# Performance work log

Hardware: AMD Instinct MI355X
Metric: run time of the kernel (lower is better)

## Reference

```python
import jax, jax.numpy as jnp
import numpy as np

NUM_BLOCKS = 2
RES_LAYERS = 10
RC, DC, SC, EC, OC, GC = 32, 32, 1024, 512, 256, 5
RF = NUM_BLOCKS * (2 ** RES_LAYERS - 1)  # receptive/residual field = 2046


def _conv(x, w, dil, pad_left):
    # x: (N, C, L), w: (O, I, K). Causal: left pad only (equivalent to
    # torch padding=d followed by slicing off the last d samples).
    return jax.lax.conv_general_dilated(
        x, w, window_strides=(1,), padding=[(pad_left, 0)],
        rhs_dilation=(dil,), dimension_numbers=('NCH', 'OIH', 'NCH'))


def setup_inputs() -> dict:
    key = jax.random.key(0)
    ks = jax.random.split(key, 13)
    B, L = 2, 8192
    nl = NUM_BLOCKS * RES_LAYERS
    s = lambda k, shape, sc: (jax.random.normal(k, shape, jnp.float32) * sc)
    return {
        'inputs': s(ks[0], (B, 256, L), 1.0),
        'conditioning': s(ks[1], (B, GC), 1.0),
        'input_w': s(ks[2], (RC, 256, 1), 0.06),
        'filter_w': s(ks[3], (nl, DC, RC, 2), 0.12),
        'gate_w': s(ks[4], (nl, DC, RC, 2), 0.12),
        'res_w': s(ks[5], (nl, RC, DC, 1), 0.17),
        'split_w': s(ks[6], (nl, SC, DC, 1), 0.17),
        'gcf_w': s(ks[7], (nl, 1, GC), 0.3),
        'gcs_w': s(ks[8], (nl, 1, GC), 0.3),
        'f1_w': s(ks[9], (EC, SC, 1), 0.03),
        'f1_b': jnp.zeros((EC,), jnp.float32),
        'f2_w': s(ks[10], (OC, EC, 1), 0.04),
        'f2_b': jnp.zeros((OC,), jnp.float32),
    }


def reference(inputs, conditioning, input_w, filter_w, gate_w, res_w,
              split_w, gcf_w, gcs_w, f1_w, f1_b, f2_w, f2_b):
    L = inputs.shape[2]
    tgt = L - RF  # target_length
    res = _conv(inputs, input_w, 1, 0)  # (B, RC, L)
    final = jnp.zeros((inputs.shape[0], SC, tgt), inputs.dtype)
    for b in range(NUM_BLOCKS):
        for l in range(RES_LAYERS):
            i = b * RES_LAYERS + l
            d = 2 ** l
            f = _conv(res, filter_w[i], d, d)  # causal dilated, length L
            g = _conv(res, gate_w[i], d, d)
            # global conditioning: Linear(GC,1) -> per-batch scalar, broadcast
            gc_f = (conditioning @ gcf_w[i].T)[:, None, :]  # (B,1,1)
            gc_g = (conditioning @ gcs_w[i].T)[:, None, :]
            out = jnp.tanh(f + gc_f) * jax.nn.sigmoid(g + gc_g)
            res = _conv(out, res_w[i], 1, 0) + res
            final = final + _conv(out, split_w[i], 1, 0)[:, :, -tgt:]
    x = jax.nn.relu(final)
    x = _conv(x, f1_w, 1, 0) + f1_b[None, :, None]
    x = jax.nn.relu(x)
    x = _conv(x, f2_w, 1, 0) + f2_b[None, :, None]
    n, c, ln = x.shape
    return jnp.transpose(x, (0, 2, 1)).reshape(n * ln, c)
```

## Files before the change

kernel.cpp:

```cpp
#include <hip/hip_runtime.h>
#include <hip/hip_bf16.h>
#include <cstddef>

#define Bc   2
#define Lc   8192
#define TGT  6146
#define NL   20
#define RCc  32
#define DCc  32
#define SCc  1024
#define ECc  512
#define OCc  256
#define KTOT (NL * DCc)
#define TTILES 49

typedef __attribute__((ext_vector_type(4))) float f32x4;
typedef __attribute__((ext_vector_type(8))) short bf16x8;
typedef __attribute__((ext_vector_type(4))) int i32x4;
typedef __attribute__((ext_vector_type(2))) int i32x2;

typedef __attribute__((address_space(1))) void* as1v;
typedef __attribute__((address_space(3))) void* as3v;

__device__ inline bf16x8 cvt8(const float4* p) {
    float4 a = p[0], b = p[1];
    union { bf16x8 v; __hip_bfloat16 h[8]; } u;
    u.h[0] = __float2bfloat16(a.x); u.h[1] = __float2bfloat16(a.y);
    u.h[2] = __float2bfloat16(a.z); u.h[3] = __float2bfloat16(a.w);
    u.h[4] = __float2bfloat16(b.x); u.h[5] = __float2bfloat16(b.y);
    u.h[6] = __float2bfloat16(b.z); u.h[7] = __float2bfloat16(b.w);
    return u.v;
}

__global__ __launch_bounds__(256) void prep_kernel(
    const float* __restrict__ x,
    const float* __restrict__ iw,
    float* __restrict__ res_out,
    const float* __restrict__ split_w,
    const float* __restrict__ f1_w,
    const float* __restrict__ f2_w,
    const float* __restrict__ filt,
    const float* __restrict__ gate,
    const float* __restrict__ resw,
    __hip_bfloat16* __restrict__ Wp1,
    __hip_bfloat16* __restrict__ Wp2,
    __hip_bfloat16* __restrict__ Wp3,
    __hip_bfloat16* __restrict__ wfgp,
    __hip_bfloat16* __restrict__ wrp,
    int npack)
{
    __shared__ float ws[32][256];
    __shared__ float xs[64][64];
    int tid = threadIdx.x;

    if ((int)blockIdx.x < npack) {
        int idx = blockIdx.x * 256 + tid;
        const int N1 = SCc * KTOT, N2 = ECc * SCc, N3 = OCc * ECc, N4 = NL * 64 * 64;
        if (idx < N1) {
            int m = idx / KTOT, k = idx % KTOT;
            int i = k >> 5, c = k & 31;
            Wp1[idx] = __float2bfloat16(split_w[((size_t)i * SCc + m) * DCc + c]);
            return;
        }
        idx -= N1;
        if (idx < N2) { Wp2[idx] = __float2bfloat16(f1_w[idx]); return; }
        idx -= N2;
        if (idx < N3) { Wp3[idx] = __float2bfloat16(f2_w[idx]); return; }
        idx -= N3;
        if (idx < N4) {
            int li = idx / 4096, r = idx % 4096;
            int m = r >> 6, k = r & 63;
            int tap = k >> 5, ic = k & 31;
            float v = (m < 32) ? filt[(size_t)li * 2048 + (m * 32 + ic) * 2 + tap]
                               : gate[(size_t)li * 2048 + ((m - 32) * 32 + ic) * 2 + tap];
            int slot = (k >> 3) ^ (m & 7);
            wfgp[((size_t)li * 64 + m) * 64 + slot * 8 + (k & 7)] = __float2bfloat16(v);
            if (r < 2048) {
                int m2 = r >> 6;
                float v2 = (k < 32) ? resw[(size_t)li * 1024 + m2 * 32 + k] : 0.f;
                wrp[((size_t)li * 32 + m2) * 64 + slot * 8 + (k & 7)] = __float2bfloat16(v2);
            }
        }
        return;
    }

    int bid = blockIdx.x - npack;
    int b   = bid >> 7;
    int t0  = (bid & 127) * 64;

    for (int idx = tid; idx < 32 * 256; idx += 256)
        ws[idx >> 8][idx & 255] = iw[idx];

    int tl = tid & 63, qq = tid >> 6, oc0 = qq * 8;
    float acc[8] = {};

    for (int icc = 0; icc < 4; ++icc) {
        __syncthreads();
        for (int idx = tid; idx < 64 * 64; idx += 256) {
            int icl = idx >> 6, tll = idx & 63;
            xs[icl][tll] = x[((size_t)b * 256 + icc * 64 + icl) * Lc + t0 + tll];
        }
        __syncthreads();
        for (int icl = 0; icl < 64; icl += 4) {
            float x0 = xs[icl][tl], x1 = xs[icl + 1][tl];
            float x2 = xs[icl + 2][tl], x3 = xs[icl + 3][tl];
#pragma unroll
            for (int j = 0; j < 8; ++j) {
                const float4 w4 = *(const float4*)&ws[oc0 + j][icc * 64 + icl];
                acc[j] += w4.x * x0 + w4.y * x1 + w4.z * x2 + w4.w * x3;
            }
        }
    }
#pragma unroll
    for (int j = 0; j < 8; ++j)
        res_out[((size_t)b * 32 + oc0 + j) * Lc + t0 + tl] = acc[j];
}

__global__ __launch_bounds__(512) void layer_group5(
    const float* __restrict__ res_in,
    float* __restrict__ res_out,
    __hip_bfloat16* __restrict__ outsT,
    const __hip_bfloat16* __restrict__ wfgp,
    const __hip_bfloat16* __restrict__ wrp,
    const float* __restrict__ cond,
    const float* __restrict__ gcf_w,
    const float* __restrict__ gcs_w,
    int l0)
{
    constexpr int W = 96, H = 32, NT = 6;
    __shared__ __align__(16) float resL[W * 36];
    __shared__ __align__(16) unsigned short OsL[W * 40];
    __shared__ __align__(16) i32x4 Wf[2][64 * 8];
    __shared__ __align__(16) i32x4 Wrs[2][32 * 8];

    int tid  = threadIdx.x;
    int b    = blockIdx.y;
    int t0   = blockIdx.x * 64;
    int lane = tid & 63, wid = tid >> 6;
    int r15  = lane & 15, q = lane >> 4;

    const float* rb = res_in + (size_t)b * 32 * Lc;
    for (int idx = tid; idx < W * 32; idx += 512) {
        int ch = idx / W, tl = idx % W;
        int tg = t0 - H + tl;
        resL[tl * 36 + ch] = (tg >= 0) ? rb[(size_t)ch * Lc + tg] : 0.f;
    }

    auto issueW = [&](int bufi, int li2) {
        const __hip_bfloat16* wfg = wfgp + (size_t)li2 * 4096;
        const __hip_bfloat16* wrl = wrp  + (size_t)li2 * 2048;
        __builtin_amdgcn_global_load_lds(
            (as1v)(void*)((const i32x4*)wfg + wid * 64 + lane),
            (as3v)(void*)&Wf[bufi][wid * 64], 16, 0, 0);
        if (wid < 4)
            __builtin_amdgcn_global_load_lds(
                (as1v)(void*)((const i32x4*)wrl + wid * 64 + lane),
                (as3v)(void*)&Wrs[bufi][wid * 64], 16, 0, 0);
    };
    issueW(0, l0);

#pragma unroll
    for (int i = 0; i < 5; ++i) {
        const int cur = i & 1;
        int li = l0 + i;
        int d  = 1 << i;

        float gf = 0.f, gg = 0.f;
#pragma unroll
        for (int c = 0; c < 5; ++c) {
            gf += gcf_w[li * 5 + c] * cond[b * 5 + c];
            gg += gcs_w[li * 5 + c] * cond[b * 5 + c];
        }
        __syncthreads();
        if (i + 1 < 5) issueW(cur ^ 1, li + 1);

        const bf16x8* Wv = (const bf16x8*)Wf[cur];
        for (int tt = wid; tt < NT; tt += 8) {
            int ct0 = tt * 16;
            int srow0 = ct0 + r15 - d; if (srow0 < 0) srow0 = 0;
            int srow1 = ct0 + r15;
            bf16x8 a0 = cvt8((const float4*)&resL[srow0 * 36 + q * 8]);
            bf16x8 a1 = cvt8((const float4*)&resL[srow1 * 36 + q * 8]);
            int sg0 = q ^ (r15 & 7), sg1 = (4 + q) ^ (r15 & 7);
            f32x4 acc[4] = {};
#pragma unroll
            for (int fj = 0; fj < 4; ++fj)
                acc[fj] = __builtin_amdgcn_mfma_f32_16x16x32_bf16(
                    a0, Wv[(fj * 16 + r15) * 8 + sg0], acc[fj], 0, 0, 0);
#pragma unroll
            for (int fj = 0; fj < 4; ++fj)
                acc[fj] = __builtin_amdgcn_mfma_f32_16x16x32_bf16(
                    a1, Wv[(fj * 16 + r15) * 8 + sg1], acc[fj], 0, 0, 0);
#pragma unroll
            for (int fj = 0; fj < 2; ++fj) {
#pragma unroll
                for (int r = 0; r < 4; ++r) {
                    float F = acc[fj][r] + gf;
                    float G = acc[fj + 2][r] + gg;
                    float th  = 1.f - 2.f / (__expf(2.f * F) + 1.f);
                    float sgm = 1.f / (1.f + __expf(-G));
                    float o   = th * sgm;
                    int col = ct0 + q * 4 + r;
                    int ch  = fj * 16 + r15;
                    __hip_bfloat16 ob = __float2bfloat16(o);
                    OsL[col * 40 + ch] = *(unsigned short*)&ob;
                }
            }
        }
        __syncthreads();

        {
            int row = tid >> 3, chunk = tid & 7;
            int tg = t0 + row;
            if (tg >= Lc - TGT) {
                i32x2 v = *(const i32x2*)&OsL[(H + row) * 40 + chunk * 4];
                *(i32x2*)(outsT + ((size_t)(b * TGT + tg - (Lc - TGT))) * KTOT
                          + li * 32 + chunk * 4) = v;
            }
        }

        const bf16x8* Rv = (const bf16x8*)Wrs[cur];
        const bf16x8* Ov = (const bf16x8*)OsL;
        for (int tt = wid; tt < NT; tt += 8) {
            int ct0 = tt * 16;
            bf16x8 ao = Ov[(ct0 + r15) * 5 + q];
            int sg = q ^ (r15 & 7);
            f32x4 racc[2] = {};
#pragma unroll
            for (int fj = 0; fj < 2; ++fj)
                racc[fj] = __builtin_amdgcn_mfma_f32_16x16x32_bf16(
                    ao, Rv[(fj * 16 + r15) * 8 + sg], racc[fj], 0, 0, 0);
#pragma unroll
            for (int fj = 0; fj < 2; ++fj)
#pragma unroll
                for (int r = 0; r < 4; ++r) {
                    int col = ct0 + q * 4 + r;
                    int ch  = fj * 16 + r15;
                    if (t0 + col - H >= 0)
                        resL[col * 36 + ch] += racc[fj][r];
                }
        }
    }
    __syncthreads();

    {
        int ch = tid >> 4, t4 = (tid & 15) * 4;
        float v[4];
#pragma unroll
        for (int j = 0; j < 4; ++j) v[j] = resL[(H + t4 + j) * 36 + ch];
        float* ro = res_out + ((size_t)(b * 32) + ch) * Lc + t0 + t4;
        *(float4*)ro = make_float4(v[0], v[1], v[2], v[3]);
    }
}

template <bool LASTHALF>
__global__ __launch_bounds__(512) void layer_groupS(
    const float* __restrict__ res_in,
    float* __restrict__ res_out,
    __hip_bfloat16* __restrict__ outsT,
    const __hip_bfloat16* __restrict__ wfgp,
    const __hip_bfloat16* __restrict__ wrp,
    const float* __restrict__ cond,
    const float* __restrict__ gcf_w,
    const float* __restrict__ gcs_w,
    int l0)
{
    constexpr int W = 96, H = 32, NT = 6, S = 32;
    __shared__ __align__(16) float resL[W * 36];
    __shared__ __align__(16) unsigned short OsL[W * 40];
    __shared__ __align__(16) i32x4 Wf[2][64 * 8];
    __shared__ __align__(16) i32x4 Wrs[2][32 * 8];

    int tid  = threadIdx.x;
    int b    = blockIdx.y;
    int r    = blockIdx.x & 31;
    int c0   = (blockIdx.x >> 5) * 64;
    int lane = tid & 63, wid = tid >> 6;
    int r15  = lane & 15, q = lane >> 4;

    const float* rb = res_in + (size_t)b * 32 * Lc;
    for (int idx = tid; idx < W * 32; idx += 512) {
        int ch = idx / W, col = idx % W;
        int cj = c0 + col - H;
        resL[col * 36 + ch] = (cj >= 0) ? rb[(size_t)ch * Lc + r + S * cj] : 0.f;
    }

    auto issueW = [&](int bufi, int li2) {
        const __hip_bfloat16* wfg = wfgp + (size_t)li2 * 4096;
        const __hip_bfloat16* wrl = wrp  + (size_t)li2 * 2048;
        __builtin_amdgcn_global_load_lds(
            (as1v)(void*)((const i32x4*)wfg + wid * 64 + lane),
            (as3v)(void*)&Wf[bufi][wid * 64], 16, 0, 0);
        if (wid < 4)
            __builtin_amdgcn_global_load_lds(
                (as1v)(void*)((const i32x4*)wrl + wid * 64 + lane),
                (as3v)(void*)&Wrs[bufi][wid * 64], 16, 0, 0);
    };
    issueW(0, l0);

#pragma unroll
    for (int i = 0; i < 5; ++i) {
        const int cur = i & 1;
        int li = l0 + i;
        int dc = 1 << i;

        float gf = 0.f, gg = 0.f;
#pragma unroll
        for (int c = 0; c < 5; ++c) {
            gf += gcf_w[li * 5 + c] * cond[b * 5 + c];
            gg += gcs_w[li * 5 + c] * cond[b * 5 + c];
        }
        __syncthreads();
        if (i + 1 < 5) issueW(cur ^ 1, li + 1);

        const bf16x8* Wv = (const bf16x8*)Wf[cur];
        for (int tt = wid; tt < NT; tt += 8) {
            int ct0 = tt * 16;
            int srow0 = ct0 + r15 - dc; if (srow0 < 0) srow0 = 0;
            int srow1 = ct0 + r15;
            bf16x8 a0 = cvt8((const float4*)&resL[srow0 * 36 + q * 8]);
            bf16x8 a1 = cvt8((const float4*)&resL[srow1 * 36 + q * 8]);
            int sg0 = q ^ (r15 & 7), sg1 = (4 + q) ^ (r15 & 7);
            f32x4 acc[4] = {};
#pragma unroll
            for (int fj = 0; fj < 4; ++fj)
                acc[fj] = __builtin_amdgcn_mfma_f32_16x16x32_bf16(
                    a0, Wv[(fj * 16 + r15) * 8 + sg0], acc[fj], 0, 0, 0);
#pragma unroll
            for (int fj = 0; fj < 4; ++fj)
                acc[fj] = __builtin_amdgcn_mfma_f32_16x16x32_bf16(
                    a1, Wv[(fj * 16 + r15) * 8 + sg1], acc[fj], 0, 0, 0);
#pragma unroll
            for (int fj = 0; fj < 2; ++fj) {
#pragma unroll
                for (int rr = 0; rr < 4; ++rr) {
                    float F = acc[fj][rr] + gf;
                    float G = acc[fj + 2][rr] + gg;
                    float th  = 1.f - 2.f / (__expf(2.f * F) + 1.f);
                    float sgm = 1.f / (1.f + __expf(-G));
                    float o   = th * sgm;
                    int col = ct0 + q * 4 + rr;
                    int ch  = fj * 16 + r15;
                    __hip_bfloat16 ob = __float2bfloat16(o);
                    OsL[col * 40 + ch] = *(unsigned short*)&ob;
                }
            }
        }
        __syncthreads();

        {
            int row = tid >> 3, chunk = tid & 7;
            int t = r + S * (c0 + row);
            if (t >= Lc - TGT) {
                i32x2 v = *(const i32x2*)&OsL[(H + row) * 40 + chunk * 4];
                *(i32x2*)(outsT + ((size_t)(b * TGT + t - (Lc - TGT))) * KTOT
                          + li * 32 + chunk * 4) = v;
            }
        }

        if (!(LASTHALF && i == 4)) {
            const bf16x8* Rv = (const bf16x8*)Wrs[cur];
            const bf16x8* Ov = (const bf16x8*)OsL;
            for (int tt = wid; tt < NT; tt += 8) {
                int ct0 = tt * 16;
                bf16x8 ao = Ov[(ct0 + r15) * 5 + q];
                int sg = q ^ (r15 & 7);
                f32x4 racc[2] = {};
#pragma unroll
                for (int fj = 0; fj < 2; ++fj)
                    racc[fj] = __builtin_amdgcn_mfma_f32_16x16x32_bf16(
                        ao, Rv[(fj * 16 + r15) * 8 + sg], racc[fj], 0, 0, 0);
#pragma unroll
                for (int fj = 0; fj < 2; ++fj)
#pragma unroll
                    for (int rr = 0; rr < 4; ++rr) {
                        int col = ct0 + q * 4 + rr;
                        int ch  = fj * 16 + r15;
                        if (c0 + col - H >= 0)
                            resL[col * 36 + ch] += racc[fj][rr];
                    }
            }
        }
    }

    if (!LASTHALF) {
        __syncthreads();
        int ch = tid >> 4, t4 = (tid & 15) * 4;
#pragma unroll
        for (int j = 0; j < 4; ++j) {
            int t = r + S * (c0 + t4 + j);
            res_out[((size_t)(b * 32) + ch) * Lc + t] = resL[(H + t4 + j) * 36 + ch];
        }
    }
}

template <bool RELU_OUT, bool OUT_BF16, int NKT>
__global__ __launch_bounds__(256) void gemm_mfma(
    const __hip_bfloat16* __restrict__ X,
    const __hip_bfloat16* __restrict__ W,
    const float* __restrict__ bias,
    void* __restrict__ Y,
    int M, int MB)
{
    constexpr int K = NKT * 64;
    __shared__ __align__(16) char smem[65536];
    i32x4* Xs0 = (i32x4*)smem;
    i32x4* Ws0 = (i32x4*)(smem + 16384);
    i32x4* Xs1 = (i32x4*)(smem + 32768);
    i32x4* Ws1 = (i32x4*)(smem + 49152);

    int nwg  = gridDim.x;
    int orig = blockIdx.x;
    int q8 = nwg >> 3, r8 = nwg & 7;
    int xcd = orig & 7, loc = orig >> 3;
    int wgid = (xcd < r8 ? xcd * (q8 + 1) : r8 * (q8 + 1) + (xcd - r8) * q8) + loc;
    int mi  = wgid % MB;
    int byy = wgid / MB;
    int b   = byy / TTILES;
    int t0  = (byy % TTILES) * 128;
    int m0  = mi * 128;

    int tid = threadIdx.x;
    int lane = tid & 63, wid = tid >> 6;
    int wy = wid >> 1, wx = wid & 1;
    int r15 = lane & 15, q = lane >> 4;

    int subrow = lane >> 3;
    int g      = (lane & 7) ^ subrow;
    const __hip_bfloat16* xp[4];
    const __hip_bfloat16* wp[4];
#pragma unroll
    for (int i = 0; i < 4; ++i) {
        int r = wid * 32 + i * 8 + subrow;
        int xrow = t0 + r; if (xrow > TGT - 1) xrow = TGT - 1;
        xp[i] = X + ((size_t)(b * TGT + xrow)) * K + g * 8;
        wp[i] = W + ((size_t)(m0 + r)) * K + g * 8;
    }

    f32x4 acc[4][4] = {};

#define STAGE(XB, WB)                                                          \
    {                                                                          \
        _Pragma("unroll")                                                      \
        for (int i = 0; i < 4; ++i) {                                          \
            __builtin_amdgcn_global_load_lds((as1v)(void*)xp[i],               \
                (as3v)(void*)&XB[(wid * 4 + i) * 64], 16, 0, 0);               \
            __builtin_amdgcn_global_load_lds((as1v)(void*)wp[i],               \
                (as3v)(void*)&WB[(wid * 4 + i) * 64], 16, 0, 0);               \
            xp[i] += 64; wp[i] += 64;                                          \
        }                                                                      \
    }

    auto compute = [&](const i32x4* Xb, const i32x4* Wb) {
        const bf16x8* Xv = (const bf16x8*)Xb;
        const bf16x8* Wv = (const bf16x8*)Wb;
#pragma unroll
        for (int kk = 0; kk < 2; ++kk) {
            int sg = (kk * 4 + q) ^ (r15 & 7);
            bf16x8 af[4], bw[4];
#pragma unroll
            for (int ft = 0; ft < 4; ++ft)
                af[ft] = Xv[(wy * 64 + ft * 16 + r15) * 8 + sg];
#pragma unroll
            for (int fj = 0; fj < 4; ++fj)
                bw[fj] = Wv[(wx * 64 + fj * 16 + r15) * 8 + sg];
#pragma unroll
            for (int ft = 0; ft < 4; ++ft)
#pragma unroll
                for (int fj = 0; fj < 4; ++fj)
                    acc[ft][fj] = __builtin_amdgcn_mfma_f32_16x16x32_bf16(
                        af[ft], bw[fj], acc[ft][fj], 0, 0, 0);
        }
    };

    STAGE(Xs0, Ws0);

#pragma unroll
    for (int kt2 = 0; kt2 < NKT; kt2 += 2) {
        STAGE(Xs1, Ws1);
        asm volatile("s_waitcnt vmcnt(8)" ::: "memory");
        __builtin_amdgcn_s_barrier();
        __builtin_amdgcn_sched_barrier(0);
        __builtin_amdgcn_s_setprio(1);
        compute(Xs0, Ws0);
        __builtin_amdgcn_s_setprio(0);
        __builtin_amdgcn_sched_barrier(0);
        __builtin_amdgcn_s_barrier();

        if (kt2 + 2 < NKT) {
            STAGE(Xs0, Ws0);
            asm volatile("s_waitcnt vmcnt(8)" ::: "memory");
        } else {
            asm volatile("s_waitcnt vmcnt(0)" ::: "memory");
        }
        __builtin_amdgcn_s_barrier();
        __builtin_amdgcn_sched_barrier(0);
        __builtin_amdgcn_s_setprio(1);
        compute(Xs1, Ws1);
        __builtin_amdgcn_s_setprio(0);
        __builtin_amdgcn_sched_barrier(0);
        __builtin_amdgcn_s_barrier();
    }
#undef STAGE

    if (OUT_BF16) {
        __hip_bfloat16* Eb = (__hip_bfloat16*)smem;
#pragma unroll
        for (int ft = 0; ft < 4; ++ft) {
#pragma unroll
            for (int r = 0; r < 4; ++r) {
                int tl = wy * 64 + ft * 16 + q * 4 + r;
#pragma unroll
                for (int fj = 0; fj < 4; ++fj) {
                    int ml = wx * 64 + fj * 16 + r15;
                    float v = acc[ft][fj][r];
                    if (bias) v += bias[m0 + ml];
                    if (RELU_OUT) v = fmaxf(v, 0.f);
                    Eb[tl * 136 + ml] = __float2bfloat16(v);
                }
            }
        }
        __syncthreads();
        int row = tid >> 1, half = tid & 1;
        int t = t0 + row;
        if (t < TGT) {
            __hip_bfloat16* dst = (__hip_bfloat16*)Y + ((size_t)(b * TGT + t)) * M + m0 + half * 64;
            const __hip_bfloat16* src = Eb + row * 136 + half * 64;
#pragma unroll
            for (int k = 0; k < 8; ++k)
                ((i32x4*)dst)[k] = ((const i32x4*)src)[k];
        }
    } else {
#pragma unroll
        for (int ft = 0; ft < 4; ++ft) {
#pragma unroll
            for (int r = 0; r < 4; ++r) {
                int t = t0 + wy * 64 + ft * 16 + q * 4 + r;
                if (t < TGT) {
                    size_t rowoff = ((size_t)(b * TGT + t)) * M;
#pragma unroll
                    for (int fj = 0; fj < 4; ++fj) {
                        int m = m0 + wx * 64 + fj * 16 + r15;
                        float v = acc[ft][fj][r];
                        if (bias) v += bias[m];
                        if (RELU_OUT) v = fmaxf(v, 0.f);
                        ((float*)Y)[rowoff + m] = v;
                    }
                }
            }
        }
    }
}

extern "C" void kernel_launch(void* const* d_in, const int* in_sizes, int n_in,
                              void* d_out, int out_size, void* d_ws, size_t ws_size,
                              hipStream_t stream)
{
    const float* inputs   = (const float*)d_in[0];
    const float* cond     = (const float*)d_in[1];
    const float* input_w  = (const float*)d_in[2];
    const float* filter_w = (const float*)d_in[3];
    const float* gate_w   = (const float*)d_in[4];
    const float* res_w    = (const float*)d_in[5];
    const float* split_w  = (const float*)d_in[6];
    const float* gcf_w    = (const float*)d_in[7];
    const float* gcs_w    = (const float*)d_in[8];
    const float* f1_w     = (const float*)d_in[9];
    const float* f1_b     = (const float*)d_in[10];
    const float* f2_w     = (const float*)d_in[11];
    const float* f2_b     = (const float*)d_in[12];
    float* out = (float*)d_out;

    char* wsb = (char*)d_ws;
    const size_t RES_B   = (size_t)Bc * RCc * Lc * 4;
    const size_t OUTS_B  = (size_t)Bc * TGT * KTOT * 2;
    const size_t FIN_B   = (size_t)Bc * TGT * SCc * 2;
    const size_t H1_B    = (size_t)Bc * TGT * ECc * 2;
    const size_t W1_B    = (size_t)SCc * KTOT * 2;
    const size_t W2_B    = (size_t)ECc * SCc * 2;
    const size_t W3_B    = (size_t)OCc * ECc * 2;
    const size_t WFG_B   = (size_t)NL * 64 * 64 * 2;
    const size_t WR_B    = (size_t)NL * 32 * 64 * 2;

    float* res0              = (float*)wsb;                   size_t off = RES_B;
    float* res1              = (float*)(wsb + off);           off += RES_B;
    __hip_bfloat16* outsT    = (__hip_bfloat16*)(wsb + off);  off += OUTS_B;
    __hip_bfloat16* finalT   = (__hip_bfloat16*)(wsb + off);  off += FIN_B;
    __hip_bfloat16* h1T      = (__hip_bfloat16*)(wsb + off);  off += H1_B;
    __hip_bfloat16* Wp1      = (__hip_bfloat16*)(wsb + off);  off += W1_B;
    __hip_bfloat16* Wp2      = (__hip_bfloat16*)(wsb + off);  off += W2_B;
    __hip_bfloat16* Wp3      = (__hip_bfloat16*)(wsb + off);  off += W3_B;
    __hip_bfloat16* wfgp     = (__hip_bfloat16*)(wsb + off);  off += WFG_B;
    __hip_bfloat16* wrp      = (__hip_bfloat16*)(wsb + off);  off += WR_B;

    {
        const int NTOT = SCc * KTOT + ECc * SCc + OCc * ECc + NL * 64 * 64;
        const int npack = (NTOT + 255) / 256;
        prep_kernel<<<npack + Bc * 128, 256, 0, stream>>>(
            inputs, input_w, res0,
            split_w, f1_w, f2_w, filter_w, gate_w, res_w,
            Wp1, Wp2, Wp3, wfgp, wrp, npack);
    }

    float* rin = res0;
    float* rout = res1;
    const dim3 lgrid(Lc / 64, Bc);
    const dim3 sgrid(128, Bc);

    layer_group5<<<lgrid, 512, 0, stream>>>(
        rin, rout, outsT, wfgp, wrp, cond, gcf_w, gcs_w, 0);
    { float* t = rin; rin = rout; rout = t; }
    layer_groupS<false><<<sgrid, 512, 0, stream>>>(
        rin, rout, outsT, wfgp, wrp, cond, gcf_w, gcs_w, 5);
    { float* t = rin; rin = rout; rout = t; }

    layer_group5<<<lgrid, 512, 0, stream>>>(
        rin, rout, outsT, wfgp, wrp, cond, gcf_w, gcs_w, 10);
    { float* t = rin; rin = rout; rout = t; }
    layer_groupS<true><<<sgrid, 512, 0, stream>>>(
        rin, rout, outsT, wfgp, wrp, cond, gcf_w, gcs_w, 15);

    gemm_mfma<true, true, 10><<<(SCc / 128) * Bc * TTILES, 256, 0, stream>>>(
        outsT, Wp1, nullptr, finalT, SCc, SCc / 128);

    gemm_mfma<true, true, 16><<<(ECc / 128) * Bc * TTILES, 256, 0, stream>>>(
        finalT, Wp2, f1_b, h1T, ECc, ECc / 128);

    gemm_mfma<false, false, 8><<<(OCc / 128) * Bc * TTILES, 256, 0, stream>>>(
        h1T, Wp3, f2_b, out, OCc, OCc / 128);
}
```

Baseline: 178.7 us.

## Fuse final two pointwise GEMMs with hidden activations kept in LDS

Replaces the separate f1 and f2 GEMM launches with one kernel. Each 512-thread workgroup computes a 64-row tile of the full 512-wide hidden layer, applies bias and ReLU, stores it as bf16 in shared memory, then multiplies it by the f2 weights. This removes the h1 round trip through global memory and one launch. In exchange it uses about 150KB of LDS per workgroup, so only one workgroup fits per CU, and the grid is just 194 workgroups.

```diff
diff --git a/kernel.cpp b/kernel.cpp
--- a/kernel.cpp
+++ b/kernel.cpp
@@ -13,6 +13,7 @@
 #define OCc  256
 #define KTOT (NL * DCc)
 #define TTILES 49
+#define T64   97
 
 typedef __attribute__((ext_vector_type(4))) float f32x4;
 typedef __attribute__((ext_vector_type(8))) short bf16x8;
@@ -552,6 +553,190 @@
     }
 }
 
+__global__ __launch_bounds__(512) void gemm_fused23(
+    const __hip_bfloat16* __restrict__ X,
+    const __hip_bfloat16* __restrict__ W2,
+    const float* __restrict__ b1,
+    const __hip_bfloat16* __restrict__ W3,
+    const float* __restrict__ b2,
+    float* __restrict__ Y)
+{
+    __shared__ __align__(16) char smem[153600];
+    i32x4* Xs[2] = { (i32x4*)smem, (i32x4*)(smem + 8192) };
+    i32x4* Ws[2] = { (i32x4*)(smem + 16384), (i32x4*)(smem + 81920) };
+    __hip_bfloat16* Hs = (__hip_bfloat16*)(smem + 16384);
+    i32x4* W3s[2] = { (i32x4*)(smem + 88064), (i32x4*)(smem + 120832) };
+
+    int nwg  = gridDim.x;
+    int orig = blockIdx.x;
+    int q8 = nwg >> 3, r8 = nwg & 7;
+    int xcd = orig & 7, loc = orig >> 3;
+    int wgid = (xcd < r8 ? xcd * (q8 + 1) : r8 * (q8 + 1) + (xcd - r8) * q8) + loc;
+    int b  = wgid / T64;
+    int t0 = (wgid % T64) * 64;
+
+    int tid = threadIdx.x;
+    int lane = tid & 63, wid = tid >> 6;
+    int r15 = lane & 15, q = lane >> 4;
+    int subrow = lane >> 3;
+    int g      = (lane & 7) ^ subrow;
+
+    int xr = wid * 8 + subrow;
+    int xrow = t0 + xr; if (xrow > TGT - 1) xrow = TGT - 1;
+    const __hip_bfloat16* xp = X + ((size_t)(b * TGT + xrow)) * SCc + g * 8;
+    const __hip_bfloat16* wp[8];
+#pragma unroll
+    for (int i = 0; i < 8; ++i)
+        wp[i] = W2 + ((size_t)((wid * 8 + i) * 8 + subrow)) * SCc + g * 8;
+
+    f32x4 acc[4][4] = {};
+
+#define STAGEA(bi)                                                             \
+    {                                                                          \
+        __builtin_amdgcn_global_load_lds((as1v)(void*)xp,                      \
+            (as3v)(void*)&Xs[bi][wid * 64], 16, 0, 0);                         \
+        xp += 64;                                                              \
+        _Pragma("unroll")                                                      \
+        for (int i = 0; i < 8; ++i) {                                          \
+            __builtin_amdgcn_global_load_lds((as1v)(void*)wp[i],               \
+                (as3v)(void*)&Ws[bi][(wid * 8 + i) * 64], 16, 0, 0);           \
+            wp[i] += 64;                                                       \
+        }                                                                      \
+    }
+
+    auto computeA = [&](const i32x4* Xb, const i32x4* Wb) {
+        const bf16x8* Xv = (const bf16x8*)Xb;
+        const bf16x8* Wv = (const bf16x8*)Wb;
+#pragma unroll
+        for (int kk = 0; kk < 2; ++kk) {
+            int sg = (kk * 4 + q) ^ (r15 & 7);
+            bf16x8 af[4], bw[4];
+#pragma unroll
+            for (int ft = 0; ft < 4; ++ft)
+                af[ft] = Xv[(ft * 16 + r15) * 8 + sg];
+#pragma unroll
+            for (int fj = 0; fj < 4; ++fj)
+                bw[fj] = Wv[(wid * 64 + fj * 16 + r15) * 8 + sg];
+#pragma unroll
+            for (int ft = 0; ft < 4; ++ft)
+#pragma unroll
+                for (int fj = 0; fj < 4; ++fj)
+                    acc[ft][fj] = __builtin_amdgcn_mfma_f32_16x16x32_bf16(
+                        af[ft], bw[fj], acc[ft][fj], 0, 0, 0);
+        }
+    };
+
+    STAGEA(0);
+#pragma unroll
+    for (int kt = 0; kt < 16; ++kt) {
+        const int cur = kt & 1;
+        if (kt + 1 < 16) {
+            STAGEA(cur ^ 1);
+            asm volatile("s_waitcnt vmcnt(9)" ::: "memory");
+        } else {
+            asm volatile("s_waitcnt vmcnt(0)" ::: "memory");
+        }
+        __builtin_amdgcn_s_barrier();
+        __builtin_amdgcn_sched_barrier(0);
+        __builtin_amdgcn_s_setprio(1);
+        computeA(Xs[cur], Ws[cur]);
+        __builtin_amdgcn_s_setprio(0);
+        __builtin_amdgcn_sched_barrier(0);
+        __builtin_amdgcn_s_barrier();
+    }
+#undef STAGEA
+
+#pragma unroll
+    for (int ft = 0; ft < 4; ++ft) {
+#pragma unroll
+        for (int r = 0; r < 4; ++r) {
+            int tl = ft * 16 + q * 4 + r;
+#pragma unroll
+            for (int fj = 0; fj < 4; ++fj) {
+                int m = wid * 64 + fj * 16 + r15;
+                float v = acc[ft][fj][r] + b1[m];
+                v = fmaxf(v, 0.f);
+                Hs[tl * 520 + m] = __float2bfloat16(v);
+            }
+        }
+    }
+
+    const __hip_bfloat16* w3p[4];
+#pragma unroll
+    for (int i = 0; i < 4; ++i)
+        w3p[i] = W3 + ((size_t)((wid * 4 + i) * 8 + subrow)) * ECc + g * 8;
+
+#define STAGEB(bi)                                                             \
+    {                                                                          \
+        _Pragma("unroll")                                                      \
+        for (int i = 0; i < 4; ++i) {                                          \
+            __builtin_amdgcn_global_load_lds((as1v)(void*)w3p[i],              \
+                (as3v)(void*)&W3s[bi][(wid * 4 + i) * 64], 16, 0, 0);          \
+            w3p[i] += 64;                                                      \
+        }                                                                      \
+    }
+
+    STAGEB(0);
+    __syncthreads();
+
+    f32x4 accB[4][2] = {};
+
+#pragma unroll
+    for (int kt = 0; kt < 8; ++kt) {
+        const int cur = kt & 1;
+        if (kt + 1 < 8) {
+            STAGEB(cur ^ 1);
+            asm volatile("s_waitcnt vmcnt(4)" ::: "memory");
+        } else {
+            asm volatile("s_waitcnt vmcnt(0)" ::: "memory");
+        }
+        __builtin_amdgcn_s_barrier();
+        __builtin_amdgcn_sched_barrier(0);
+        __builtin_amdgcn_s_setprio(1);
+        {
+            const bf16x8* Wv = (const bf16x8*)W3s[cur];
+#pragma unroll
+            for (int kk = 0; kk < 2; ++kk) {
+                int gk = kt * 8 + kk * 4 + q;
+                int sg = (kk * 4 + q) ^ (r15 & 7);
+                bf16x8 af[4], bw[2];
+#pragma unroll
+                for (int ft = 0; ft < 4; ++ft)
+                    af[ft] = *(const bf16x8*)&Hs[(ft * 16 + r15) * 520 + gk * 8];
+#pragma unroll
+                for (int fj = 0; fj < 2; ++fj)
+                    bw[fj] = Wv[(wid * 32 + fj * 16 + r15) * 8 + sg];
+#pragma unroll
+                for (int ft = 0; ft < 4; ++ft)
+#pragma unroll
+                    for (int fj = 0; fj < 2; ++fj)
+                        accB[ft][fj] = __builtin_amdgcn_mfma_f32_16x16x32_bf16(
+                            af[ft], bw[fj], accB[ft][fj], 0, 0, 0);
+            }
+        }
+        __builtin_amdgcn_s_setprio(0);
+        __builtin_amdgcn_sched_barrier(0);
+        __builtin_amdgcn_s_barrier();
+    }
+#undef STAGEB
+
+#pragma unroll
+    for (int ft = 0; ft < 4; ++ft) {
+#pragma unroll
+        for (int r = 0; r < 4; ++r) {
+            int t = t0 + ft * 16 + q * 4 + r;
+            if (t < TGT) {
+                size_t rowoff = ((size_t)(b * TGT + t)) * OCc;
+#pragma unroll
+                for (int fj = 0; fj < 2; ++fj) {
+                    int m = wid * 32 + fj * 16 + r15;
+                    Y[rowoff + m] = accB[ft][fj][r] + b2[m];
+                }
+            }
+        }
+    }
+}
+
 extern "C" void kernel_launch(void* const* d_in, const int* in_sizes, int n_in,
                               void* d_out, int out_size, void* d_ws, size_t ws_size,
                               hipStream_t stream)
@@ -575,7 +760,6 @@
     const size_t RES_B   = (size_t)Bc * RCc * Lc * 4;
     const size_t OUTS_B  = (size_t)Bc * TGT * KTOT * 2;
     const size_t FIN_B   = (size_t)Bc * TGT * SCc * 2;
-    const size_t H1_B    = (size_t)Bc * TGT * ECc * 2;
     const size_t W1_B    = (size_t)SCc * KTOT * 2;
     const size_t W2_B    = (size_t)ECc * SCc * 2;
     const size_t W3_B    = (size_t)OCc * ECc * 2;
@@ -586,7 +770,6 @@
     float* res1              = (float*)(wsb + off);           off += RES_B;
     __hip_bfloat16* outsT    = (__hip_bfloat16*)(wsb + off);  off += OUTS_B;
     __hip_bfloat16* finalT   = (__hip_bfloat16*)(wsb + off);  off += FIN_B;
-    __hip_bfloat16* h1T      = (__hip_bfloat16*)(wsb + off);  off += H1_B;
     __hip_bfloat16* Wp1      = (__hip_bfloat16*)(wsb + off);  off += W1_B;
     __hip_bfloat16* Wp2      = (__hip_bfloat16*)(wsb + off);  off += W2_B;
     __hip_bfloat16* Wp3      = (__hip_bfloat16*)(wsb + off);  off += W3_B;
@@ -613,7 +796,6 @@
     layer_groupS<false><<<sgrid, 512, 0, stream>>>(
         rin, rout, outsT, wfgp, wrp, cond, gcf_w, gcs_w, 5);
     { float* t = rin; rin = rout; rout = t; }
-
     layer_group5<<<lgrid, 512, 0, stream>>>(
         rin, rout, outsT, wfgp, wrp, cond, gcf_w, gcs_w, 10);
     { float* t = rin; rin = rout; rout = t; }
@@ -623,9 +805,6 @@
     gemm_mfma<true, true, 10><<<(SCc / 128) * Bc * TTILES, 256, 0, stream>>>(
         outsT, Wp1, nullptr, finalT, SCc, SCc / 128);
 
-    gemm_mfma<true, true, 16><<<(ECc / 128) * Bc * TTILES, 256, 0, stream>>>(
-        finalT, Wp2, f1_b, h1T, ECc, ECc / 128);
-
-    gemm_mfma<false, false, 8><<<(OCc / 128) * Bc * TTILES, 256, 0, stream>>>(
-        h1T, Wp3, f2_b, out, OCc, OCc / 128);
+    gemm_fused23<<<Bc * T64, 512, 0, stream>>>(
+        finalT, Wp2, f1_b, Wp3, f2_b, out);
 }
```

New measurement: 166.8 us. 6.7% less time.
